# Kernel optimization log

Hardware: AMD Instinct MI355X
Metric: run time of the kernel (lower is better)

Reference implementation:

```python
import jax, jax.numpy as jnp
import numpy as np

B, S, IN, HID = 128, 512, 1024, 1024
CHI, KAPPA, DT = 0.638, 0.35, 0.01
NC = 6  # num zeta corridors


def setup_inputs() -> dict:
    key = jax.random.key(0)
    ks = jax.random.split(key, 10)
    def rn(k, shp, s=0.02):
        return jax.random.normal(k, shp, dtype=jnp.float32) * s
    return {
        "x": jax.random.normal(ks[0], (B, S, IN), dtype=jnp.float32),
        "W_gates": rn(ks[1], (IN + HID, 4 * HID)),  # fused [i|f|g|o] gate weights
        "b_gates": jnp.zeros((4 * HID,), jnp.float32),
        "mirror_W": rn(ks[2], (HID, HID)),
        "mirror_b": jnp.zeros((HID,), jnp.float32),
        "curv_W1": rn(ks[3], (HID, HID // 2)),
        "curv_b1": jnp.zeros((HID // 2,), jnp.float32),
        "curv_W2": rn(ks[4], (HID // 2, 1)),
        "curv_b2": jnp.zeros((1,), jnp.float32),
        "evo_W": rn(ks[5], (HID, HID)),
        "evo_b": jnp.zeros((HID,), jnp.float32),
        "zeta_w": jax.random.normal(ks[6], (NC,), dtype=jnp.float32),
        "zeta_p": jax.random.normal(ks[7], (NC,), dtype=jnp.float32),
    }


def _zeta_loss(zw, zp):
    # Per recurrent step seq_len==1 so s-points are (sigma=0.5, t=-2) for every batch
    # element; the functional-equation loss is therefore a single scalar independent
    # of the hidden state, and the mean over identical points equals that scalar.
    L = 0.2 + 0.1 * jnp.arange(NC, dtype=jnp.float32)  # corridor lengths
    s0 = jnp.complex64(0.5 - 2.0j)
    def xi(s):
        t1 = jnp.exp(-s * L)
        t2 = jax.nn.sigmoid(zp).astype(jnp.complex64) * jnp.exp(-(1.0 - s) * L)
        return jnp.sum(jax.nn.sigmoid(zw).astype(jnp.complex64) * 0.5 * (t1 + t2))
    d = xi(s0) - xi(1.0 - s0)
    return (d * jnp.conj(d)).real  # |Xi(s) - Xi(1-s)|^2


def reference(x, W_gates, b_gates, mirror_W, mirror_b,
              curv_W1, curv_b1, curv_W2, curv_b2,
              evo_W, evo_b, zeta_w, zeta_p):
    Wx, Wh = W_gates[:IN], W_gates[IN:]
    # Precompute the input contribution of all 4 gates for every timestep (one big GEMM).
    gx = jnp.einsum('bsi,ig->bsg', x, Wx) + b_gates        # [B,S,4H]
    gx = jnp.swapaxes(gx, 0, 1)                            # [S,B,4H] for scan
    h0 = jnp.zeros((x.shape[0], HID), x.dtype)
    c0 = jnp.zeros((x.shape[0], HID), x.dtype)

    def step(carry, g):
        h, c = carry
        gates = g + h @ Wh                                  # [B,4H]
        i, f, gg, o = jnp.split(gates, 4, axis=-1)
        i, f, o = jax.nn.sigmoid(i), jax.nn.sigmoid(f), jax.nn.sigmoid(o)
        gg = jnp.tanh(gg)
        c = f * c + i * gg
        # curvature coupling: scalar curvature per batch element gates an evolution step
        kap = CHI * (jax.nn.relu(c @ curv_W1 + curv_b1) @ curv_W2 + curv_b2)  # [B,1]
        c = c + DT * kap * (c @ evo_W + evo_b)
        # mirror operator + guardian threshold
        h = jnp.tanh((o * jnp.tanh(c)) @ mirror_W + mirror_b)
        h = h / (1.0 + KAPPA * jnp.abs(h))
        return (h, c), h

    (h, c), ys = jax.lax.scan(step, (h0, c0), gx)
    outputs = jnp.swapaxes(ys, 0, 1)                        # [B,S,H]
    # zeta regularization loss is identical each step, so the seq-mean equals one eval
    return outputs, h, c, _zeta_loss(zeta_w, zeta_p)
```

## Files before the change

### kernel.cpp

```cpp
#include <hip/hip_runtime.h>
#include <hip/hip_bf16.h>
#include <math.h>
#include <stdint.h>

#define B_    128
#define S_    512
#define IN_   1024
#define HID_  1024
#define CHI_  0.638f
#define KAPPA_ 0.35f
#define DT_   0.01f
#define CH    32
#define NCHUNK (S_/CH)

#define OUT_H 67108864
#define OUT_C 67239936
#define OUT_Z 67371008

#define WS_CNT   0
#define WS_KP    2048
#define WS_HBF   6144
#define WS_CF32  268288
#define WS_STATE_BYTES 792576
#define WS_CBF   792576
#define WS_MBF   1054720
#define WS_WGT   1316864
#define WS_EVOT  18094080
#define WS_MIRT  20191232
#define WS_C1T   22288384
#define WS_XBF   23336960
#define WS_GXC   31725568

using s16x8 = __attribute__((ext_vector_type(8))) short;
using s16x4 = __attribute__((ext_vector_type(4))) short;
using f32x4 = __attribute__((ext_vector_type(4))) float;
typedef unsigned long long u64;

static __device__ __forceinline__ short f2bf(float x){
  unsigned int u = __float_as_uint(x);
  u = (u + 0x7FFFu + ((u >> 16) & 1u)) >> 16;
  return (short)u;
}
static __device__ __forceinline__ float b2f(short s){
  return __uint_as_float(((unsigned int)(unsigned short)s) << 16);
}
static __device__ __forceinline__ float sigf(float x){
  return 1.f / (1.f + __expf(-x));
}
static __device__ __forceinline__ float tanhf_(float x){
  return 1.f - 2.f / (__expf(2.f * x) + 1.f);
}
static __device__ __forceinline__ f32x4 mfma16(s16x8 a, s16x8 b, f32x4 c){
  return __builtin_amdgcn_mfma_f32_16x16x32_bf16(a, b, c, 0, 0, 0);
}

static __device__ __forceinline__ u64 ld_coh_u64(const void* p){
  return __hip_atomic_load((const u64*)p, __ATOMIC_RELAXED, __HIP_MEMORY_SCOPE_AGENT);
}
static __device__ __forceinline__ void st_coh_u64(void* p, u64 v){
  __hip_atomic_store((u64*)p, v, __ATOMIC_RELAXED, __HIP_MEMORY_SCOPE_AGENT);
}
static __device__ __forceinline__ float ld_coh_f32(const float* p){
  return __hip_atomic_load(p, __ATOMIC_RELAXED, __HIP_MEMORY_SCOPE_AGENT);
}
static __device__ __forceinline__ void st_coh_f32(float* p, float v){
  __hip_atomic_store(p, v, __ATOMIC_RELAXED, __HIP_MEMORY_SCOPE_AGENT);
}
static __device__ __forceinline__ unsigned ld_coh_u32(const unsigned* p){
  return __hip_atomic_load(p, __ATOMIC_RELAXED, __HIP_MEMORY_SCOPE_AGENT);
}
static __device__ __forceinline__ void st_coh_u32(unsigned* p, unsigned v){
  __hip_atomic_store(p, v, __ATOMIC_RELAXED, __HIP_MEMORY_SCOPE_AGENT);
}
static __device__ __forceinline__ void at_add_f32(float* p, float v){
  __hip_atomic_fetch_add(p, v, __ATOMIC_RELAXED, __HIP_MEMORY_SCOPE_AGENT);
}
static __device__ __forceinline__ s16x8 ld_coh16B(const short* p){
  union { u64 q[2]; s16x8 v; } u;
  u.q[0] = ld_coh_u64(p);
  u.q[1] = ld_coh_u64(p + 4);
  return u.v;
}

static __device__ __forceinline__ void gbar(unsigned* arr, int n, unsigned gen){
  asm volatile("s_waitcnt vmcnt(0)" ::: "memory");
  __syncthreads();
  if (threadIdx.x < 32){
    if (threadIdx.x == 0) st_coh_u32(arr + n, gen);
    unsigned v = ld_coh_u32(arr + threadIdx.x);
    while (!__all(v >= gen)){
      __builtin_amdgcn_s_sleep(2);
      v = ld_coh_u32(arr + threadIdx.x);
    }
  }
  __syncthreads();
}

__global__ void transpose_bf(const float* __restrict__ in, short* __restrict__ out,
                             int R, int C){
  __shared__ float tile[32][33];
  int c0 = blockIdx.x * 32, r0 = blockIdx.y * 32;
  int tc = threadIdx.x & 31, tr = threadIdx.x >> 5;
  #pragma unroll
  for (int i = 0; i < 4; i++){
    int r = tr + i * 8;
    tile[r][tc] = in[(size_t)(r0 + r) * C + (c0 + tc)];
  }
  __syncthreads();
  #pragma unroll
  for (int i = 0; i < 4; i++){
    int cc = tr + i * 8;
    out[(size_t)(c0 + cc) * R + (r0 + tc)] = f2bf(tile[tc][cc]);
  }
}

__global__ void conv_x(const float* __restrict__ x, short* __restrict__ xbf, int t0){
  int rb = blockIdx.x;
  int tl = rb >> 7, b = rb & 127;
  const float* src = x + ((size_t)b * S_ + (t0 + tl)) * (size_t)IN_;
  short* dst = xbf + (size_t)rb * IN_;
  int i = threadIdx.x * 4;
  float4 v = *(const float4*)(src + i);
  s16x4 o; o[0]=f2bf(v.x); o[1]=f2bf(v.y); o[2]=f2bf(v.z); o[3]=f2bf(v.w);
  *(s16x4*)(dst + i) = o;
}

__global__ __launch_bounds__(256, 2) void gemm_gx(const short* __restrict__ Ax,
                                                  const short* __restrict__ wgT,
                                                  short* __restrict__ gxc){
  __shared__ short As[128 * 32];
  __shared__ short Bs[128 * 32];
  const int tid = threadIdx.x, w = tid >> 6, l = tid & 63;
  const int wm = w & 1, wn = w >> 1;
  const int bn = blockIdx.x, bm = blockIdx.y;
  const int lc = l & 15, kg = l >> 4;
  f32x4 acc[4][4];
  #pragma unroll
  for (int i = 0; i < 4; i++)
    #pragma unroll
    for (int j = 0; j < 4; j++) acc[i][j] = f32x4{0.f, 0.f, 0.f, 0.f};

  const int srow = tid >> 1;
  const int so = (tid & 1) * 32;
  const short* ga = Ax  + (size_t)(bm * 128 + srow) * 1024 + (so >> 1);
  const short* gb = wgT + (size_t)(bn * 128 + srow) * 2048 + (so >> 1);
  const int sp0 = srow * 64 + ((so)      ^ ((srow & 3) << 4));
  const int sp1 = srow * 64 + ((so + 16) ^ ((srow & 3) << 4));

  uint4 ra0, ra1, rb0, rb1;
  auto LD = [&](int kt){
    ra0 = *(const uint4*)(ga + kt * 32);
    ra1 = *(const uint4*)(ga + kt * 32 + 8);
    rb0 = *(const uint4*)(gb + kt * 32);
    rb1 = *(const uint4*)(gb + kt * 32 + 8);
  };
  LD(0);
  for (int kt = 0; kt < 32; ++kt){
    __syncthreads();
    *(uint4*)((char*)As + sp0) = ra0;
    *(uint4*)((char*)As + sp1) = ra1;
    *(uint4*)((char*)Bs + sp0) = rb0;
    *(uint4*)((char*)Bs + sp1) = rb1;
    __syncthreads();
    if (kt + 1 < 32) LD(kt + 1);
    s16x8 af[4], bfr[4];
    #pragma unroll
    for (int mf = 0; mf < 4; ++mf){
      int row = wm * 64 + mf * 16 + lc;
      af[mf] = *(const s16x8*)((const char*)As + row * 64 + ((kg * 16) ^ ((row & 3) << 4)));
    }
    #pragma unroll
    for (int nf = 0; nf < 4; ++nf){
      int row = wn * 64 + nf * 16 + lc;
      bfr[nf] = *(const s16x8*)((const char*)Bs + row * 64 + ((kg * 16) ^ ((row & 3) << 4)));
    }
    #pragma unroll
    for (int mf = 0; mf < 4; ++mf)
      #pragma unroll
      for (int nf = 0; nf < 4; ++nf)
        acc[mf][nf] = mfma16(af[mf], bfr[nf], acc[mf][nf]);
  }
  #pragma unroll
  for (int mf = 0; mf < 4; ++mf){
    #pragma unroll
    for (int nf = 0; nf < 4; ++nf){
      int gg = wm * 4 + mf;
      int gc = bn * 128 + wn * 64 + nf * 16 + lc;
      s16x4 pk;
      #pragma unroll
      for (int r = 0; r < 4; r++) pk[r] = f2bf(acc[mf][nf][r]);
      *(s16x4*)(gxc + (((size_t)bm * 8 + gg) * 4096 + gc) * 16 + kg * 4) = pk;
    }
  }
}

struct cpx { double r, i; };
static __device__ cpx cexp_(cpx z){ double e = exp(z.r); return {e * cos(z.i), e * sin(z.i)}; }
static __device__ cpx xi_(double sr, double si, const float* zw, const float* zp){
  cpx acc{0.0, 0.0};
  for (int i = 0; i < 6; i++){
    double L = 0.2 + 0.1 * i;
    double sw = 1.0 / (1.0 + exp(-(double)zw[i]));
    double sp = 1.0 / (1.0 + exp(-(double)zp[i]));
    cpx t1 = cexp_({-sr * L, -si * L});
    cpx t2 = cexp_({-(1.0 - sr) * L, si * L});
    acc.r += sw * 0.5 * (t1.r + sp * t2.r);
    acc.i += sw * 0.5 * (t1.i + sp * t2.i);
  }
  return acc;
}
__global__ void zeta_k(const float* __restrict__ zw, const float* __restrict__ zp,
                       float* __restrict__ dz){
  if (threadIdx.x == 0 && blockIdx.x == 0){
    cpx a = xi_(0.5, -2.0, zw, zp);
    cpx b = xi_(0.5,  2.0, zw, zp);
    double dr = a.r - b.r, di = a.i - b.i;
    dz[0] = (float)(dr * dr + di * di);
  }
}

#define RSLOT(slot, j) ((char*)red + (slot) * 8192 + (size_t)l * 128 + (((j) * 16) ^ ((l & 7) << 4)))

__global__ __launch_bounds__(512, 2) void scan_k(
    const short* __restrict__ wgT, const short* __restrict__ evoT,
    const short* __restrict__ mirT, const short* __restrict__ c1T,
    const short* __restrict__ gxc,
    const float* __restrict__ bg,  const float* __restrict__ evob,
    const float* __restrict__ mirb, const float* __restrict__ cb1,
    const float* __restrict__ cw2, const float* __restrict__ cb2,
    short* __restrict__ hbf, short* __restrict__ cbf, short* __restrict__ mbf,
    float* __restrict__ cf32, float* __restrict__ kp,
    unsigned int* __restrict__ cnt, float* __restrict__ dout, int t0)
{
  const int tid = threadIdx.x;
  const int w = tid >> 6, l = tid & 63;
  const int lc = l & 15, kg = l >> 4;
  const int bi = blockIdx.x;
  const int g = bi >> 5, n = bi & 31;
  unsigned* arr = cnt + g * 64;

  __shared__ float red[4][64][32];
  __shared__ float gatesL[4][16][33];
  __shared__ float eL[16][33];
  __shared__ float kpart[16][8];
  __shared__ float kapL[16];
  __shared__ short stL[16][32];
  __shared__ float hfL[16][32];

  const short* hG = hbf + (size_t)g * 16384;
  const short* cG = cbf + (size_t)g * 16384;
  const short* mG = mbf + (size_t)g * 16384;
  float* kpg = kp + g * 128;

  const int pl = (tid & 127) >> 1, ph = tid & 1;
  const size_t poff = (size_t)(n * 64 + pl) * 8 + ph * 4;
  const int psr = pl & 15, psc = (pl >> 4) * 8 + ph * 4;

  const int orow = tid >> 5, ocolL = tid & 31;
  const int ocol = n * 32 + ocolL;
  const size_t oidx = (size_t)(g * 16 + orow) * HID_ + ocol;
  float c_state = cf32[oidx];
  float o_reg = 0.f;
  float bgv[4];
  #pragma unroll
  for (int q = 0; q < 4; q++) bgv[q] = bg[q * 1024 + ocol];
  const float cb2v = cb2[0];

  const short* bqp[4][2];
  #pragma unroll
  for (int q = 0; q < 4; q++)
    #pragma unroll
    for (int cf = 0; cf < 2; cf++)
      bqp[q][cf] = wgT + (size_t)(q * 1024 + n * 32 + cf * 16 + lc) * 2048 + 1024 + w * 128 + kg * 8;
  const short* bevo0 = evoT + (size_t)(n * 32 + lc) * 1024 + w * 128 + kg * 8;
  const short* bevo1 = bevo0 + 16 * 1024;
  const short* bcur  = c1T + (size_t)(n * 16 + lc) * 1024 + w * 128 + kg * 8;
  const short* bmir0 = mirT + (size_t)(n * 32 + lc) * 1024 + w * 128 + kg * 8;
  const short* bmir1 = bmir0 + 16 * 1024;
  const float eb0 = evob[n * 32 + lc], eb1 = evob[n * 32 + 16 + lc];
  const float c1bv = cb1[n * 16 + lc], c2wv = cw2[n * 16 + lc];
  const float mb0 = mirb[n * 32 + lc], mb1 = mirb[n * 32 + 16 + lc];

  unsigned gen = (unsigned)t0 * 4;

  for (int lt = 0; lt < CH; ++lt){
    const int t = t0 + lt;

    float gxv[4];
    #pragma unroll
    for (int q = 0; q < 4; q++)
      gxv[q] = b2f(gxc[(((size_t)lt * 8 + g) * 4096 + q * 1024 + ocol) * 16 + orow]);

    {
      f32x4 acc[4][2];
      #pragma unroll
      for (int q = 0; q < 4; q++){ acc[q][0] = f32x4{0,0,0,0}; acc[q][1] = f32x4{0,0,0,0}; }
      #pragma unroll
      for (int ks = 0; ks < 4; ++ks){
        int kq = w * 4 + ks;
        s16x8 a = ld_coh16B(hG + (size_t)(kq * 64 + l) * 8);
        #pragma unroll
        for (int q = 0; q < 4; q++){
          s16x8 b0 = *(const s16x8*)(bqp[q][0] + ks * 32);
          s16x8 b1 = *(const s16x8*)(bqp[q][1] + ks * 32);
          acc[q][0] = mfma16(a, b0, acc[q][0]);
          acc[q][1] = mfma16(a, b1, acc[q][1]);
        }
      }
      f32x4* accf = (f32x4*)acc;
      if (w >= 4){
        #pragma unroll
        for (int j = 0; j < 8; j++) *(f32x4*)RSLOT(w - 4, j) = accf[j];
      }
      __syncthreads();
      if (w < 4){
        #pragma unroll
        for (int j = 0; j < 8; j++) accf[j] += *(const f32x4*)RSLOT(w, j);
      }
      __syncthreads();
      if (w == 2 || w == 3){
        #pragma unroll
        for (int j = 0; j < 8; j++) *(f32x4*)RSLOT(w - 2, j) = accf[j];
      }
      __syncthreads();
      if (w < 2){
        #pragma unroll
        for (int j = 0; j < 8; j++) accf[j] += *(const f32x4*)RSLOT(w, j);
      }
      __syncthreads();
      if (w == 1){
        #pragma unroll
        for (int j = 0; j < 8; j++) *(f32x4*)RSLOT(0, j) = accf[j];
      }
      __syncthreads();
      if (w == 0){
        #pragma unroll
        for (int j = 0; j < 8; j++) accf[j] += *(const f32x4*)RSLOT(0, j);
        #pragma unroll
        for (int q = 0; q < 4; q++)
          #pragma unroll
          for (int cf = 0; cf < 2; cf++)
            #pragma unroll
            for (int r = 0; r < 4; r++)
              gatesL[q][kg * 4 + r][cf * 16 + lc] = acc[q][cf][r];
      }
      __syncthreads();
      float pre[4];
      #pragma unroll
      for (int q = 0; q < 4; q++)
        pre[q] = gatesL[q][orow][ocolL] + bgv[q] + gxv[q];
      float ii = sigf(pre[0]), ff = sigf(pre[1]);
      float gt = tanhf_(pre[2]);
      o_reg = sigf(pre[3]);
      c_state = ff * c_state + ii * gt;
      stL[orow][ocolL] = f2bf(c_state);
      __syncthreads();
      if (tid < 128)
        st_coh_u64((void*)(cG + poff), *(const u64*)&stL[psr][psc]);
    }
    gbar(arr, n, ++gen);

    {
      f32x4 e0{0,0,0,0}, e1{0,0,0,0}, cv{0,0,0,0};
      #pragma unroll
      for (int ks = 0; ks < 4; ++ks){
        int kq = w * 4 + ks;
        s16x8 a = ld_coh16B(cG + (size_t)(kq * 64 + l) * 8);
        s16x8 b0 = *(const s16x8*)(bevo0 + ks * 32);
        s16x8 b1 = *(const s16x8*)(bevo1 + ks * 32);
        s16x8 bc = *(const s16x8*)(bcur + ks * 32);
        e0 = mfma16(a, b0, e0);
        e1 = mfma16(a, b1, e1);
        cv = mfma16(a, bc, cv);
      }
      if (w >= 4){
        *(f32x4*)RSLOT(w - 4, 0) = e0; *(f32x4*)RSLOT(w - 4, 1) = e1; *(f32x4*)RSLOT(w - 4, 2) = cv;
      }
      __syncthreads();
      if (w < 4){
        e0 += *(const f32x4*)RSLOT(w, 0); e1 += *(const f32x4*)RSLOT(w, 1); cv += *(const f32x4*)RSLOT(w, 2);
      }
      __syncthreads();
      if (w == 2 || w == 3){
        *(f32x4*)RSLOT(w - 2, 0) = e0; *(f32x4*)RSLOT(w - 2, 1) = e1; *(f32x4*)RSLOT(w - 2, 2) = cv;
      }
      __syncthreads();
      if (w < 2){
        e0 += *(const f32x4*)RSLOT(w, 0); e1 += *(const f32x4*)RSLOT(w, 1); cv += *(const f32x4*)RSLOT(w, 2);
      }
      __syncthreads();
      if (w == 1){
        *(f32x4*)RSLOT(0, 0) = e0; *(f32x4*)RSLOT(0, 1) = e1; *(f32x4*)RSLOT(0, 2) = cv;
      }
      __syncthreads();
      if (w == 0){
        e0 += *(const f32x4*)RSLOT(0, 0); e1 += *(const f32x4*)RSLOT(0, 1); cv += *(const f32x4*)RSLOT(0, 2);
        #pragma unroll
        for (int r = 0; r < 4; r++){
          eL[kg * 4 + r][lc]      = e0[r] + eb0;
          eL[kg * 4 + r][16 + lc] = e1[r] + eb1;
          float v = fmaxf(cv[r] + c1bv, 0.f) * c2wv;
          v += __shfl_xor(v, 1); v += __shfl_xor(v, 2);
          v += __shfl_xor(v, 4); v += __shfl_xor(v, 8);
          if (lc == 0)
            at_add_f32(kpg + (kg * 4 + r) * 8 + (n >> 2), v);
        }
      }
    }
    gbar(arr, n, ++gen);

    {
      if (tid < 128)
        kpart[tid >> 3][tid & 7] = ld_coh_f32(kpg + tid);
      __syncthreads();
      if (tid < 16){
        float s = 0.f;
        #pragma unroll
        for (int j = 0; j < 8; j++) s += kpart[tid][j];
        kapL[tid] = CHI_ * (s + cb2v);
      }
      __syncthreads();
      {
        float e = eL[orow][ocolL];
        c_state = c_state + DT_ * kapL[orow] * e;
        float mm = o_reg * tanhf_(c_state);
        stL[orow][ocolL] = f2bf(mm);
        if (t == S_ - 1) dout[OUT_C + oidx] = c_state;
        if (lt == CH - 1) cf32[oidx] = c_state;
      }
      __syncthreads();
      if (tid < 128)
        st_coh_u64((void*)(mG + poff), *(const u64*)&stL[psr][psc]);
    }
    gbar(arr, n, ++gen);

    {
      f32x4 h0{0,0,0,0}, h1{0,0,0,0};
      #pragma unroll
      for (int ks = 0; ks < 4; ++ks){
        int kq = w * 4 + ks;
        s16x8 a = ld_coh16B(mG + (size_t)(kq * 64 + l) * 8);
        s16x8 b0 = *(const s16x8*)(bmir0 + ks * 32);
        s16x8 b1 = *(const s16x8*)(bmir1 + ks * 32);
        h0 = mfma16(a, b0, h0);
        h1 = mfma16(a, b1, h1);
      }
      if (w >= 4){ *(f32x4*)RSLOT(w - 4, 0) = h0; *(f32x4*)RSLOT(w - 4, 1) = h1; }
      __syncthreads();
      if (w < 4){ h0 += *(const f32x4*)RSLOT(w, 0); h1 += *(const f32x4*)RSLOT(w, 1); }
      __syncthreads();
      if (w == 2 || w == 3){ *(f32x4*)RSLOT(w - 2, 0) = h0; *(f32x4*)RSLOT(w - 2, 1) = h1; }
      __syncthreads();
      if (w < 2){ h0 += *(const f32x4*)RSLOT(w, 0); h1 += *(const f32x4*)RSLOT(w, 1); }
      __syncthreads();
      if (w == 1){ *(f32x4*)RSLOT(0, 0) = h0; *(f32x4*)RSLOT(0, 1) = h1; }
      __syncthreads();
      if (w == 0){
        h0 += *(const f32x4*)RSLOT(0, 0); h1 += *(const f32x4*)RSLOT(0, 1);
        #pragma unroll
        for (int cf = 0; cf < 2; cf++){
          #pragma unroll
          for (int r = 0; r < 4; r++){
            int row = kg * 4 + r;
            float hv = tanhf_((cf ? h1[r] : h0[r]) + (cf ? mb1 : mb0));
            hv = hv / (1.f + KAPPA_ * fabsf(hv));
            hfL[row][cf * 16 + lc] = hv;
            stL[row][cf * 16 + lc] = f2bf(hv);
          }
        }
      }
      __syncthreads();
      {
        float hv = hfL[orow][ocolL];
        dout[(size_t)(g * 16 + orow) * 524288 + (size_t)t * 1024 + ocol] = hv;
        if (t == S_ - 1) dout[OUT_H + oidx] = hv;
      }
      if (tid < 128)
        st_coh_u64((void*)(hG + poff), *(const u64*)&stL[psr][psc]);
      if (n == 0 && tid >= 128 && tid < 256)
        st_coh_f32(kpg + (tid - 128), 0.f);
    }
    gbar(arr, n, ++gen);
  }
}

extern "C" void kernel_launch(void* const* d_in, const int* in_sizes, int n_in,
                              void* d_out, int out_size, void* d_ws, size_t ws_size,
                              hipStream_t stream)
{
  (void)in_sizes; (void)n_in; (void)out_size; (void)ws_size;
  const float* x   = (const float*)d_in[0];
  const float* Wg  = (const float*)d_in[1];
  const float* bg  = (const float*)d_in[2];
  const float* miW = (const float*)d_in[3];
  const float* mib = (const float*)d_in[4];
  const float* c1W = (const float*)d_in[5];
  const float* c1b = (const float*)d_in[6];
  const float* c2W = (const float*)d_in[7];
  const float* c2b = (const float*)d_in[8];
  const float* evW = (const float*)d_in[9];
  const float* evb = (const float*)d_in[10];
  const float* zw  = (const float*)d_in[11];
  const float* zp  = (const float*)d_in[12];
  float* out = (float*)d_out;
  char* ws = (char*)d_ws;

  unsigned int* cnt = (unsigned int*)(ws + WS_CNT);
  float* kpb  = (float*)(ws + WS_KP);
  short* hbf  = (short*)(ws + WS_HBF);
  float* cf32 = (float*)(ws + WS_CF32);
  short* cbf  = (short*)(ws + WS_CBF);
  short* mbf  = (short*)(ws + WS_MBF);
  short* wgT  = (short*)(ws + WS_WGT);
  short* evoT = (short*)(ws + WS_EVOT);
  short* mirT = (short*)(ws + WS_MIRT);
  short* c1T  = (short*)(ws + WS_C1T);
  short* xbf  = (short*)(ws + WS_XBF);
  short* gxc  = (short*)(ws + WS_GXC);

  hipMemsetAsync(ws, 0, WS_STATE_BYTES, stream);

  transpose_bf<<<dim3(4096/32, 2048/32), 256, 0, stream>>>(Wg,  wgT, 2048, 4096);
  transpose_bf<<<dim3(1024/32, 1024/32), 256, 0, stream>>>(evW, evoT, 1024, 1024);
  transpose_bf<<<dim3(1024/32, 1024/32), 256, 0, stream>>>(miW, mirT, 1024, 1024);
  transpose_bf<<<dim3(512/32, 1024/32),  256, 0, stream>>>(c1W, c1T, 1024, 512);

  zeta_k<<<1, 64, 0, stream>>>(zw, zp, out + OUT_Z);

  for (int ch = 0; ch < NCHUNK; ++ch){
    conv_x<<<dim3(CH * 128), 256, 0, stream>>>(x, xbf, ch * CH);
    gemm_gx<<<dim3(32, CH), 256, 0, stream>>>(xbf, wgT, gxc);
    scan_k<<<dim3(256), 512, 0, stream>>>(wgT, evoT, mirT, c1T, gxc,
                                          bg, evb, mib, c1b, c2W, c2b,
                                          hbf, cbf, mbf, cf32, kpb,
                                          cnt, out, ch * CH);
  }
}
```

Baseline: 11.95 ms.

## Halve scan workgroups so each block owns 64 hidden columns

```diff
diff --git a/kernel.cpp b/kernel.cpp
--- a/kernel.cpp
+++ b/kernel.cpp
@@ -85,12 +85,13 @@
 static __device__ __forceinline__ void gbar(unsigned* arr, int n, unsigned gen){
   asm volatile("s_waitcnt vmcnt(0)" ::: "memory");
   __syncthreads();
-  if (threadIdx.x < 32){
+  if (threadIdx.x < 64){
     if (threadIdx.x == 0) st_coh_u32(arr + n, gen);
-    unsigned v = ld_coh_u32(arr + threadIdx.x);
+    unsigned v = gen;
+    if (threadIdx.x < 16) v = ld_coh_u32(arr + threadIdx.x);
     while (!__all(v >= gen)){
       __builtin_amdgcn_s_sleep(2);
-      v = ld_coh_u32(arr + threadIdx.x);
+      if (threadIdx.x < 16) v = ld_coh_u32(arr + threadIdx.x);
     }
   }
   __syncthreads();
@@ -221,6 +222,25 @@
 
 #define RSLOT(slot, j) ((char*)red + (slot) * 8192 + (size_t)l * 128 + (((j) * 16) ^ ((l & 7) << 4)))
 
+#define LADDER(NP, pay)                                                        \
+  if (w >= 4){ _Pragma("unroll")                                               \
+    for (int j = 0; j < (NP); j++) *(f32x4*)RSLOT(w - 4, j) = (pay)[j]; }      \
+  __syncthreads();                                                             \
+  if (w < 4){ _Pragma("unroll")                                                \
+    for (int j = 0; j < (NP); j++) (pay)[j] += *(const f32x4*)RSLOT(w, j); }   \
+  __syncthreads();                                                             \
+  if (w == 2 || w == 3){ _Pragma("unroll")                                     \
+    for (int j = 0; j < (NP); j++) *(f32x4*)RSLOT(w - 2, j) = (pay)[j]; }      \
+  __syncthreads();                                                             \
+  if (w < 2){ _Pragma("unroll")                                                \
+    for (int j = 0; j < (NP); j++) (pay)[j] += *(const f32x4*)RSLOT(w, j); }   \
+  __syncthreads();                                                             \
+  if (w == 1){ _Pragma("unroll")                                               \
+    for (int j = 0; j < (NP); j++) *(f32x4*)RSLOT(0, j) = (pay)[j]; }          \
+  __syncthreads();                                                             \
+  if (w == 0){ _Pragma("unroll")                                               \
+    for (int j = 0; j < (NP); j++) (pay)[j] += *(const f32x4*)RSLOT(0, j); }
+
 __global__ __launch_bounds__(512, 2) void scan_k(
     const short* __restrict__ wgT, const short* __restrict__ evoT,
     const short* __restrict__ mirT, const short* __restrict__ c1T,
@@ -236,174 +256,170 @@
   const int w = tid >> 6, l = tid & 63;
   const int lc = l & 15, kg = l >> 4;
   const int bi = blockIdx.x;
-  const int g = bi >> 5, n = bi & 31;
+  const int g = bi >> 4, n = bi & 15;
   unsigned* arr = cnt + g * 64;
 
   __shared__ float red[4][64][32];
-  __shared__ float gatesL[4][16][33];
-  __shared__ float eL[16][33];
+  __shared__ float gatesL[4][16][65];
+  __shared__ float eL[16][65];
   __shared__ float kpart[16][8];
   __shared__ float kapL[16];
-  __shared__ short stL[16][32];
-  __shared__ float hfL[16][32];
+  __shared__ short stL[16][64];
+  __shared__ float hfL[16][64];
 
   const short* hG = hbf + (size_t)g * 16384;
   const short* cG = cbf + (size_t)g * 16384;
   const short* mG = mbf + (size_t)g * 16384;
   float* kpg = kp + g * 128;
 
-  const int pl = (tid & 127) >> 1, ph = tid & 1;
-  const size_t poff = (size_t)(n * 64 + pl) * 8 + ph * 4;
-  const int psr = pl & 15, psc = (pl >> 4) * 8 + ph * 4;
+  const int pq = (tid >> 7) & 1, pu = tid & 127;
+  const int pl = pu >> 1, ph = pu & 1;
+  const size_t poff = (size_t)((2 * n + pq) * 64 + pl) * 8 + ph * 4;
+  const int psr = pl & 15, psc = pq * 32 + (pl >> 4) * 8 + ph * 4;
 
   const int orow = tid >> 5, ocolL = tid & 31;
-  const int ocol = n * 32 + ocolL;
-  const size_t oidx = (size_t)(g * 16 + orow) * HID_ + ocol;
-  float c_state = cf32[oidx];
-  float o_reg = 0.f;
-  float bgv[4];
-  #pragma unroll
-  for (int q = 0; q < 4; q++) bgv[q] = bg[q * 1024 + ocol];
+  const int ocol0 = n * 64 + ocolL, ocol1 = ocol0 + 32;
+  const size_t oidx0 = (size_t)(g * 16 + orow) * HID_ + ocol0;
+  const size_t oidx1 = oidx0 + 32;
+  float c_state0 = cf32[oidx0], c_state1 = cf32[oidx1];
+  float o_reg0 = 0.f, o_reg1 = 0.f;
+  float bgv0[4], bgv1[4];
+  #pragma unroll
+  for (int q = 0; q < 4; q++){
+    bgv0[q] = bg[q * 1024 + ocol0];
+    bgv1[q] = bg[q * 1024 + ocol1];
+  }
   const float cb2v = cb2[0];
 
-  const short* bqp[4][2];
-  #pragma unroll
-  for (int q = 0; q < 4; q++)
-    #pragma unroll
-    for (int cf = 0; cf < 2; cf++)
-      bqp[q][cf] = wgT + (size_t)(q * 1024 + n * 32 + cf * 16 + lc) * 2048 + 1024 + w * 128 + kg * 8;
-  const short* bevo0 = evoT + (size_t)(n * 32 + lc) * 1024 + w * 128 + kg * 8;
-  const short* bevo1 = bevo0 + 16 * 1024;
-  const short* bcur  = c1T + (size_t)(n * 16 + lc) * 1024 + w * 128 + kg * 8;
-  const short* bmir0 = mirT + (size_t)(n * 32 + lc) * 1024 + w * 128 + kg * 8;
-  const short* bmir1 = bmir0 + 16 * 1024;
-  const float eb0 = evob[n * 32 + lc], eb1 = evob[n * 32 + 16 + lc];
-  const float c1bv = cb1[n * 16 + lc], c2wv = cw2[n * 16 + lc];
-  const float mb0 = mirb[n * 32 + lc], mb1 = mirb[n * 32 + 16 + lc];
+  const short* bqA  = wgT + (size_t)(n * 64 + lc) * 2048 + 1024 + w * 128 + kg * 8;
+  const short* bevo = evoT + (size_t)(n * 64 + lc) * 1024 + w * 128 + kg * 8;
+  const short* bcur = c1T + (size_t)(n * 32 + lc) * 1024 + w * 128 + kg * 8;
+  const short* bmir = mirT + (size_t)(n * 64 + lc) * 1024 + w * 128 + kg * 8;
+  float ebv[4], mbv[4];
+  #pragma unroll
+  for (int cf = 0; cf < 4; cf++){
+    ebv[cf] = evob[n * 64 + cf * 16 + lc];
+    mbv[cf] = mirb[n * 64 + cf * 16 + lc];
+  }
+  float c1bv[2], c2wv[2];
+  #pragma unroll
+  for (int cc = 0; cc < 2; cc++){
+    c1bv[cc] = cb1[n * 32 + cc * 16 + lc];
+    c2wv[cc] = cw2[n * 32 + cc * 16 + lc];
+  }
 
   unsigned gen = (unsigned)t0 * 4;
 
   for (int lt = 0; lt < CH; ++lt){
     const int t = t0 + lt;
 
-    float gxv[4];
+    float gxv0[4], gxv1[4];
     #pragma unroll
-    for (int q = 0; q < 4; q++)
-      gxv[q] = b2f(gxc[(((size_t)lt * 8 + g) * 4096 + q * 1024 + ocol) * 16 + orow]);
+    for (int q = 0; q < 4; q++){
+      gxv0[q] = b2f(gxc[(((size_t)lt * 8 + g) * 4096 + q * 1024 + ocol0) * 16 + orow]);
+      gxv1[q] = b2f(gxc[(((size_t)lt * 8 + g) * 4096 + q * 1024 + ocol1) * 16 + orow]);
+    }
 
     {
-      f32x4 acc[4][2];
-      #pragma unroll
-      for (int q = 0; q < 4; q++){ acc[q][0] = f32x4{0,0,0,0}; acc[q][1] = f32x4{0,0,0,0}; }
+      f32x4 acc[16];
+      #pragma unroll
+      for (int j = 0; j < 16; j++) acc[j] = f32x4{0, 0, 0, 0};
       #pragma unroll
       for (int ks = 0; ks < 4; ++ks){
         int kq = w * 4 + ks;
         s16x8 a = ld_coh16B(hG + (size_t)(kq * 64 + l) * 8);
         #pragma unroll
-        for (int q = 0; q < 4; q++){
-          s16x8 b0 = *(const s16x8*)(bqp[q][0] + ks * 32);
-          s16x8 b1 = *(const s16x8*)(bqp[q][1] + ks * 32);
-          acc[q][0] = mfma16(a, b0, acc[q][0]);
-          acc[q][1] = mfma16(a, b1, acc[q][1]);
-        }
-      }
-      f32x4* accf = (f32x4*)acc;
-      if (w >= 4){
-        #pragma unroll
-        for (int j = 0; j < 8; j++) *(f32x4*)RSLOT(w - 4, j) = accf[j];
-      }
-      __syncthreads();
-      if (w < 4){
-        #pragma unroll
-        for (int j = 0; j < 8; j++) accf[j] += *(const f32x4*)RSLOT(w, j);
-      }
-      __syncthreads();
-      if (w == 2 || w == 3){
-        #pragma unroll
-        for (int j = 0; j < 8; j++) *(f32x4*)RSLOT(w - 2, j) = accf[j];
-      }
-      __syncthreads();
-      if (w < 2){
-        #pragma unroll
-        for (int j = 0; j < 8; j++) accf[j] += *(const f32x4*)RSLOT(w, j);
-      }
-      __syncthreads();
-      if (w == 1){
-        #pragma unroll
-        for (int j = 0; j < 8; j++) *(f32x4*)RSLOT(0, j) = accf[j];
-      }
-      __syncthreads();
-      if (w == 0){
-        #pragma unroll
-        for (int j = 0; j < 8; j++) accf[j] += *(const f32x4*)RSLOT(0, j);
-        #pragma unroll
         for (int q = 0; q < 4; q++)
           #pragma unroll
-          for (int cf = 0; cf < 2; cf++)
-            #pragma unroll
-            for (int r = 0; r < 4; r++)
-              gatesL[q][kg * 4 + r][cf * 16 + lc] = acc[q][cf][r];
-      }
-      __syncthreads();
-      float pre[4];
-      #pragma unroll
-      for (int q = 0; q < 4; q++)
-        pre[q] = gatesL[q][orow][ocolL] + bgv[q] + gxv[q];
-      float ii = sigf(pre[0]), ff = sigf(pre[1]);
-      float gt = tanhf_(pre[2]);
-      o_reg = sigf(pre[3]);
-      c_state = ff * c_state + ii * gt;
-      stL[orow][ocolL] = f2bf(c_state);
-      __syncthreads();
-      if (tid < 128)
+          for (int cf = 0; cf < 4; cf++){
+            s16x8 b = *(const s16x8*)(bqA + (size_t)(q * 1024 + cf * 16) * 2048 + ks * 32);
+            acc[q * 4 + cf] = mfma16(a, b, acc[q * 4 + cf]);
+          }
+      }
+      LADDER(8, acc);
+      if (w == 0){
+        #pragma unroll
+        for (int j = 0; j < 8; j++){
+          int q = j >> 2, cf = j & 3;
+          #pragma unroll
+          for (int r = 0; r < 4; r++)
+            gatesL[q][kg * 4 + r][cf * 16 + lc] = acc[j][r];
+        }
+      }
+      __syncthreads();
+      LADDER(8, (acc + 8));
+      if (w == 0){
+        #pragma unroll
+        for (int j = 0; j < 8; j++){
+          int q = 2 + (j >> 2), cf = j & 3;
+          #pragma unroll
+          for (int r = 0; r < 4; r++)
+            gatesL[q][kg * 4 + r][cf * 16 + lc] = acc[8 + j][r];
+        }
+      }
+      __syncthreads();
+      float pre0[4], pre1[4];
+      #pragma unroll
+      for (int q = 0; q < 4; q++){
+        pre0[q] = gatesL[q][orow][ocolL]      + bgv0[q] + gxv0[q];
+        pre1[q] = gatesL[q][orow][ocolL + 32] + bgv1[q] + gxv1[q];
+      }
+      {
+        float ii = sigf(pre0[0]), ff = sigf(pre0[1]);
+        float gt = tanhf_(pre0[2]);
+        o_reg0 = sigf(pre0[3]);
+        c_state0 = ff * c_state0 + ii * gt;
+        stL[orow][ocolL] = f2bf(c_state0);
+      }
+      {
+        float ii = sigf(pre1[0]), ff = sigf(pre1[1]);
+        float gt = tanhf_(pre1[2]);
+        o_reg1 = sigf(pre1[3]);
+        c_state1 = ff * c_state1 + ii * gt;
+        stL[orow][ocolL + 32] = f2bf(c_state1);
+      }
+      __syncthreads();
+      if (tid < 256)
         st_coh_u64((void*)(cG + poff), *(const u64*)&stL[psr][psc]);
     }
     gbar(arr, n, ++gen);
 
     {
-      f32x4 e0{0,0,0,0}, e1{0,0,0,0}, cv{0,0,0,0};
+      f32x4 pay[6];
+      #pragma unroll
+      for (int j = 0; j < 6; j++) pay[j] = f32x4{0, 0, 0, 0};
       #pragma unroll
       for (int ks = 0; ks < 4; ++ks){
         int kq = w * 4 + ks;
         s16x8 a = ld_coh16B(cG + (size_t)(kq * 64 + l) * 8);
-        s16x8 b0 = *(const s16x8*)(bevo0 + ks * 32);
-        s16x8 b1 = *(const s16x8*)(bevo1 + ks * 32);
-        s16x8 bc = *(const s16x8*)(bcur + ks * 32);
-        e0 = mfma16(a, b0, e0);
-        e1 = mfma16(a, b1, e1);
-        cv = mfma16(a, bc, cv);
-      }
-      if (w >= 4){
-        *(f32x4*)RSLOT(w - 4, 0) = e0; *(f32x4*)RSLOT(w - 4, 1) = e1; *(f32x4*)RSLOT(w - 4, 2) = cv;
-      }
-      __syncthreads();
-      if (w < 4){
-        e0 += *(const f32x4*)RSLOT(w, 0); e1 += *(const f32x4*)RSLOT(w, 1); cv += *(const f32x4*)RSLOT(w, 2);
-      }
-      __syncthreads();
-      if (w == 2 || w == 3){
-        *(f32x4*)RSLOT(w - 2, 0) = e0; *(f32x4*)RSLOT(w - 2, 1) = e1; *(f32x4*)RSLOT(w - 2, 2) = cv;
-      }
-      __syncthreads();
-      if (w < 2){
-        e0 += *(const f32x4*)RSLOT(w, 0); e1 += *(const f32x4*)RSLOT(w, 1); cv += *(const f32x4*)RSLOT(w, 2);
-      }
-      __syncthreads();
-      if (w == 1){
-        *(f32x4*)RSLOT(0, 0) = e0; *(f32x4*)RSLOT(0, 1) = e1; *(f32x4*)RSLOT(0, 2) = cv;
-      }
-      __syncthreads();
+        #pragma unroll
+        for (int cf = 0; cf < 4; cf++){
+          s16x8 b = *(const s16x8*)(bevo + (size_t)(cf * 16) * 1024 + ks * 32);
+          pay[cf] = mfma16(a, b, pay[cf]);
+        }
+        #pragma unroll
+        for (int cc = 0; cc < 2; cc++){
+          s16x8 b = *(const s16x8*)(bcur + (size_t)(cc * 16) * 1024 + ks * 32);
+          pay[4 + cc] = mfma16(a, b, pay[4 + cc]);
+        }
+      }
+      LADDER(6, pay);
       if (w == 0){
-        e0 += *(const f32x4*)RSLOT(0, 0); e1 += *(const f32x4*)RSLOT(0, 1); cv += *(const f32x4*)RSLOT(0, 2);
-        #pragma unroll
-        for (int r = 0; r < 4; r++){
-          eL[kg * 4 + r][lc]      = e0[r] + eb0;
-          eL[kg * 4 + r][16 + lc] = e1[r] + eb1;
-          float v = fmaxf(cv[r] + c1bv, 0.f) * c2wv;
-          v += __shfl_xor(v, 1); v += __shfl_xor(v, 2);
-          v += __shfl_xor(v, 4); v += __shfl_xor(v, 8);
-          if (lc == 0)
-            at_add_f32(kpg + (kg * 4 + r) * 8 + (n >> 2), v);
+        #pragma unroll
+        for (int cf = 0; cf < 4; cf++)
+          #pragma unroll
+          for (int r = 0; r < 4; r++)
+            eL[kg * 4 + r][cf * 16 + lc] = pay[cf][r] + ebv[cf];
+        #pragma unroll
+        for (int cc = 0; cc < 2; cc++){
+          #pragma unroll
+          for (int r = 0; r < 4; r++){
+            float v = fmaxf(pay[4 + cc][r] + c1bv[cc], 0.f) * c2wv[cc];
+            v += __shfl_xor(v, 1); v += __shfl_xor(v, 2);
+            v += __shfl_xor(v, 4); v += __shfl_xor(v, 8);
+            if (lc == 0)
+              at_add_f32(kpg + (kg * 4 + r) * 8 + ((n * 2 + cc) >> 2), v);
+          }
         }
       }
     }
@@ -421,48 +437,43 @@
       }
       __syncthreads();
       {
-        float e = eL[orow][ocolL];
-        c_state = c_state + DT_ * kapL[orow] * e;
-        float mm = o_reg * tanhf_(c_state);
-        stL[orow][ocolL] = f2bf(mm);
-        if (t == S_ - 1) dout[OUT_C + oidx] = c_state;
-        if (lt == CH - 1) cf32[oidx] = c_state;
-      }
-      __syncthreads();
-      if (tid < 128)
+        float kapr = kapL[orow];
+        float e0 = eL[orow][ocolL], e1 = eL[orow][ocolL + 32];
+        c_state0 = c_state0 + DT_ * kapr * e0;
+        c_state1 = c_state1 + DT_ * kapr * e1;
+        stL[orow][ocolL]      = f2bf(o_reg0 * tanhf_(c_state0));
+        stL[orow][ocolL + 32] = f2bf(o_reg1 * tanhf_(c_state1));
+        if (t == S_ - 1){ dout[OUT_C + oidx0] = c_state0; dout[OUT_C + oidx1] = c_state1; }
+        if (lt == CH - 1){ cf32[oidx0] = c_state0; cf32[oidx1] = c_state1; }
+      }
+      __syncthreads();
+      if (tid < 256)
         st_coh_u64((void*)(mG + poff), *(const u64*)&stL[psr][psc]);
     }
     gbar(arr, n, ++gen);
 
     {
-      f32x4 h0{0,0,0,0}, h1{0,0,0,0};
+      f32x4 hh[4];
+      #pragma unroll
+      for (int j = 0; j < 4; j++) hh[j] = f32x4{0, 0, 0, 0};
       #pragma unroll
       for (int ks = 0; ks < 4; ++ks){
         int kq = w * 4 + ks;
         s16x8 a = ld_coh16B(mG + (size_t)(kq * 64 + l) * 8);
-        s16x8 b0 = *(const s16x8*)(bmir0 + ks * 32);
-        s16x8 b1 = *(const s16x8*)(bmir1 + ks * 32);
-        h0 = mfma16(a, b0, h0);
-        h1 = mfma16(a, b1, h1);
-      }
-      if (w >= 4){ *(f32x4*)RSLOT(w - 4, 0) = h0; *(f32x4*)RSLOT(w - 4, 1) = h1; }
-      __syncthreads();
-      if (w < 4){ h0 += *(const f32x4*)RSLOT(w, 0); h1 += *(const f32x4*)RSLOT(w, 1); }
-      __syncthreads();
-      if (w == 2 || w == 3){ *(f32x4*)RSLOT(w - 2, 0) = h0; *(f32x4*)RSLOT(w - 2, 1) = h1; }
-      __syncthreads();
-      if (w < 2){ h0 += *(const f32x4*)RSLOT(w, 0); h1 += *(const f32x4*)RSLOT(w, 1); }
-      __syncthreads();
-      if (w == 1){ *(f32x4*)RSLOT(0, 0) = h0; *(f32x4*)RSLOT(0, 1) = h1; }
-      __syncthreads();
+        #pragma unroll
+        for (int cf = 0; cf < 4; cf++){
+          s16x8 b = *(const s16x8*)(bmir + (size_t)(cf * 16) * 1024 + ks * 32);
+          hh[cf] = mfma16(a, b, hh[cf]);
+        }
+      }
+      LADDER(4, hh);
       if (w == 0){
-        h0 += *(const f32x4*)RSLOT(0, 0); h1 += *(const f32x4*)RSLOT(0, 1);
-        #pragma unroll
-        for (int cf = 0; cf < 2; cf++){
+        #pragma unroll
+        for (int cf = 0; cf < 4; cf++){
           #pragma unroll
           for (int r = 0; r < 4; r++){
             int row = kg * 4 + r;
-            float hv = tanhf_((cf ? h1[r] : h0[r]) + (cf ? mb1 : mb0));
+            float hv = tanhf_(hh[cf][r] + mbv[cf]);
             hv = hv / (1.f + KAPPA_ * fabsf(hv));
             hfL[row][cf * 16 + lc] = hv;
             stL[row][cf * 16 + lc] = f2bf(hv);
@@ -471,14 +482,16 @@
       }
       __syncthreads();
       {
-        float hv = hfL[orow][ocolL];
-        dout[(size_t)(g * 16 + orow) * 524288 + (size_t)t * 1024 + ocol] = hv;
-        if (t == S_ - 1) dout[OUT_H + oidx] = hv;
-      }
-      if (tid < 128)
+        float hv0 = hfL[orow][ocolL], hv1 = hfL[orow][ocolL + 32];
+        size_t base = (size_t)(g * 16 + orow) * 524288 + (size_t)t * 1024;
+        dout[base + ocol0] = hv0;
+        dout[base + ocol1] = hv1;
+        if (t == S_ - 1){ dout[OUT_H + oidx0] = hv0; dout[OUT_H + oidx1] = hv1; }
+      }
+      if (tid < 256)
         st_coh_u64((void*)(hG + poff), *(const u64*)&stL[psr][psc]);
-      if (n == 0 && tid >= 128 && tid < 256)
-        st_coh_f32(kpg + (tid - 128), 0.f);
+      if (n == 0 && tid >= 256 && tid < 384)
+        st_coh_f32(kpg + (tid - 256), 0.f);
     }
     gbar(arr, n, ++gen);
   }
@@ -530,7 +543,7 @@
   for (int ch = 0; ch < NCHUNK; ++ch){
     conv_x<<<dim3(CH * 128), 256, 0, stream>>>(x, xbf, ch * CH);
     gemm_gx<<<dim3(32, CH), 256, 0, stream>>>(xbf, wgT, gxc);
-    scan_k<<<dim3(256), 512, 0, stream>>>(wgT, evoT, mirT, c1T, gxc,
+    scan_k<<<dim3(128), 512, 0, stream>>>(wgT, evoT, mirT, c1T, gxc,
                                           bg, evb, mib, c1b, c2W, c2b,
                                           hbf, cbf, mbf, cf32, kpb,
                                           cnt, out, ch * CH);
```

Result: slower. 24.57 ms (+105.5%).
